# Performance work log

Hardware: AMD Instinct MI355X
Metric: run time of the kernel (lower is better)

## Reference

```python
import jax, jax.numpy as jnp
import numpy as np

TILE = 128
NEG = -1e10


def rotate_half(x):
    half = x.shape[-1] // 2
    return jnp.concatenate([-x[..., half:], x[..., :half]], axis=-1)


def setup_inputs() -> dict:
    key = jax.random.key(0)
    ks = jax.random.split(key, 7)
    B, S, E, H, D, K = 1, 4096, 2048, 16, 128, 8
    T = S // TILE
    x = jax.random.normal(ks[0], (B, S, E), jnp.float32)
    wq = jax.random.normal(ks[1], (E, H * D), jnp.float32) * 0.02
    wk = jax.random.normal(ks[2], (E, H * D), jnp.float32) * 0.02
    wv = jax.random.normal(ks[3], (E, H * D), jnp.float32) * 0.02
    wo = jax.random.normal(ks[4], (H * D, E), jnp.float32) * 0.02
    rope_angles = jax.random.uniform(ks[5], (S, D // 2), jnp.float32)
    anchor_indices = jax.random.randint(ks[6], (B, H, T, K), 0, T).astype(jnp.int32)
    return {"x": x, "wq": wq, "wk": wk, "wv": wv, "wo": wo,
            "rope_angles": rope_angles, "anchor_indices": anchor_indices}


def reference(x, wq, wk, wv, wo, rope_angles, anchor_indices):
    B, S, E = x.shape
    D = rope_angles.shape[1] * 2          # head_dim
    H = wq.shape[1] // D                  # num_heads
    T = S // TILE                         # num_tiles
    sm_scale = 1.0 / jnp.sqrt(jnp.float32(D))

    # QKV projections -> [B, H, S, D]
    def proj(w):
        return (x @ w).reshape(B, S, H, D).transpose(0, 2, 1, 3).astype(jnp.float32)
    q, k, v = proj(wq), proj(wk), proj(wv)

    # RoPE (half-split / rotate_half format)
    cos = jnp.cos(rope_angles)[None, None]   # [1,1,S,D/2]
    sin = jnp.sin(rope_angles)[None, None]
    cos_f = jnp.concatenate([cos, cos], axis=-1)
    sin_f = jnp.concatenate([sin, sin], axis=-1)
    q = q * cos_f + rotate_half(q) * sin_f
    k = k * cos_f + rotate_half(k) * sin_f

    # Tile selection: anchor tiles + local (diagonal) tile -> [B,H,T,K+1]
    local = jnp.broadcast_to(jnp.arange(T, dtype=jnp.int32)[None, None, :, None], (B, H, T, 1))
    tile_sel = jnp.concatenate([anchor_indices, local], axis=-1)
    L = tile_sel.shape[-1] * TILE            # sparse_len
    token_idx = tile_sel[..., None] * TILE + jnp.arange(TILE, dtype=jnp.int32)[None, None, None, None, :]
    flat_idx = jnp.clip(token_idx.reshape(B, H, T, L), 0, S - 1)  # [B,H,T,L]

    # Gather selected KV tiles: [B,H,T,L,D]
    def gather(kv):
        return jnp.take_along_axis(kv, flat_idx.reshape(B, H, T * L, 1), axis=2).reshape(B, H, T, L, D)
    k_sp, v_sp = gather(k), gather(v)

    # Block-sparse attention per query tile
    q_t = q.reshape(B, H, T, TILE, D)
    logits = jnp.einsum('bhtqd,bhtkd->bhtqk', q_t, k_sp) * sm_scale
    q_pos = jnp.arange(S).reshape(T, TILE)
    future = flat_idx[:, :, :, None, :] > q_pos[None, None, :, :, None]  # causal mask on gathered keys
    logits = jnp.where(future, NEG, logits)
    w = jax.nn.softmax(logits, axis=-1)
    all_masked = jnp.all(future, axis=-1, keepdims=True)
    w = jnp.where(all_masked, 0.0, w)
    w = jnp.where(jnp.isnan(w), 0.0, w)
    out = jnp.einsum('bhtqk,bhtkd->bhtqd', w, v_sp)

    out = out.reshape(B, H, S, D).transpose(0, 2, 1, 3).reshape(B, S, H * D)
    return out @ wo
```

## Files before the change

### kernel.cpp

```cpp
#include <hip/hip_runtime.h>
#include <stdint.h>

typedef unsigned short u16;
typedef unsigned int u32;

#define S_LEN 4096
#define EMB 2048
#define NH 16
#define HD 128
#define HDTOT 2048
#define T_TILES 32
#define KANCH 8
#define SM_SCALE 0.088388347648318447f

typedef __bf16 bf16x8 __attribute__((ext_vector_type(8)));
typedef float f32x4 __attribute__((ext_vector_type(4)));

typedef const __attribute__((address_space(1))) u32 ga_u32;
typedef __attribute__((address_space(3))) u32 lds_u32;

__device__ __forceinline__ u16 f2bf(float f) {
  u32 b = __builtin_bit_cast(u32, f);
  b = (b + 0x7FFFu + ((b >> 16) & 1u)) >> 16;
  return (u16)b;
}
__device__ __forceinline__ float bf2f(u16 u) {
  return __builtin_bit_cast(float, ((u32)u) << 16);
}
__device__ __forceinline__ f32x4 mfma16(bf16x8 a, bf16x8 b, f32x4 c) {
  return __builtin_amdgcn_mfma_f32_16x16x32_bf16(a, b, c, 0, 0, 0);
}

__global__ __launch_bounds__(256) void k_convert_x(const float* __restrict__ x,
                                                   u16* __restrict__ xb) {
  int i = (blockIdx.x * 256 + threadIdx.x) * 4;
  float4 v = *(const float4*)(x + i);
  ushort4 o;
  o.x = f2bf(v.x); o.y = f2bf(v.y); o.z = f2bf(v.z); o.w = f2bf(v.w);
  *(ushort4*)(xb + i) = o;
}

__global__ __launch_bounds__(256) void k_transpose_w(
    const float* __restrict__ w0, const float* __restrict__ w1,
    const float* __restrict__ w2, const float* __restrict__ w3,
    u16* __restrict__ o0, u16* __restrict__ o1,
    u16* __restrict__ o2, u16* __restrict__ o3) {
  const float* w; u16* o;
  if (blockIdx.z == 0)      { w = w0; o = o0; }
  else if (blockIdx.z == 1) { w = w1; o = o1; }
  else if (blockIdx.z == 2) { w = w2; o = o2; }
  else                      { w = w3; o = o3; }
  __shared__ float tile[64][68];
  int n0 = blockIdx.x * 64, k0 = blockIdx.y * 64;
  int tid = threadIdx.x;
  int r = tid >> 4, cq = (tid & 15) << 2;
  for (int p = 0; p < 4; ++p) {
    float4 v = *(const float4*)(w + (size_t)(k0 + r + p * 16) * EMB + n0 + cq);
    tile[r + p * 16][cq + 0] = v.x;
    tile[r + p * 16][cq + 1] = v.y;
    tile[r + p * 16][cq + 2] = v.z;
    tile[r + p * 16][cq + 3] = v.w;
  }
  __syncthreads();
  for (int p = 0; p < 4; ++p) {
    int rn = r + p * 16;
    ushort4 u;
    u.x = f2bf(tile[cq + 0][rn]);
    u.y = f2bf(tile[cq + 1][rn]);
    u.z = f2bf(tile[cq + 2][rn]);
    u.w = f2bf(tile[cq + 3][rn]);
    *(ushort4*)(o + (size_t)(n0 + rn) * EMB + k0 + cq) = u;
  }
}

__global__ __launch_bounds__(256) void k_transpose_v(const u16* __restrict__ v,
                                                     u16* __restrict__ vt) {
  __shared__ u16 tile[64][72];
  int n0 = blockIdx.x * 64, s0 = blockIdx.y * 64;
  int tid = threadIdx.x;
  int r = tid >> 4, cq = (tid & 15) << 2;
  for (int p = 0; p < 4; ++p) {
    ushort4 u = *(const ushort4*)(v + (size_t)(s0 + r + p * 16) * HDTOT + n0 + cq);
    tile[r + p * 16][cq + 0] = u.x;
    tile[r + p * 16][cq + 1] = u.y;
    tile[r + p * 16][cq + 2] = u.z;
    tile[r + p * 16][cq + 3] = u.w;
  }
  __syncthreads();
  for (int p = 0; p < 4; ++p) {
    int rn = r + p * 16;
    ushort4 o;
    o.x = tile[cq + 0][rn];
    o.y = tile[cq + 1][rn];
    o.z = tile[cq + 2][rn];
    o.w = tile[cq + 3][rn];
    *(ushort4*)(vt + (size_t)(n0 + rn) * S_LEN + s0 + cq) = o;
  }
}

template <bool BF16OUT>
__device__ __forceinline__ void gemm_body(const u16* __restrict__ A,
                                          const u16* __restrict__ Bt,
                                          void* __restrict__ Cv,
                                          int N, int K, int m0, int n0,
                                          u16* As, u16* Bs) {
  const int tid = threadIdx.x;
  const int lane = tid & 63, wave = tid >> 6;
  const int quad = lane >> 4, l16 = lane & 15;
  const int wm = (wave >> 1) * 64, wn = (wave & 1) * 64;
  f32x4 acc[4][4] = {};

  const int flat0 = wave * 1024 + lane * 16;
  for (int kt = 0; kt < K; kt += 32) {
    for (int half = 0; half < 2; ++half) {
      int flat = flat0 + half * 4096;
      int row = flat >> 6, colb = flat & 63;
      const char* ga = (const char*)A + ((size_t)(m0 + row) * K + kt) * 2 + colb;
      const char* gb = (const char*)Bt + ((size_t)(n0 + row) * K + kt) * 2 + colb;
      int loff = wave * 1024 + half * 4096;
      __builtin_amdgcn_global_load_lds((ga_u32*)ga, (lds_u32*)((char*)As + loff), 16, 0, 0);
      __builtin_amdgcn_global_load_lds((ga_u32*)gb, (lds_u32*)((char*)Bs + loff), 16, 0, 0);
    }
    __syncthreads();
    bf16x8 af[4], bfr[4];
    for (int mt = 0; mt < 4; ++mt)
      af[mt] = *(const bf16x8*)(As + (wm + mt * 16 + l16) * 32 + quad * 8);
    for (int nt = 0; nt < 4; ++nt)
      bfr[nt] = *(const bf16x8*)(Bs + (wn + nt * 16 + l16) * 32 + quad * 8);
    for (int mt = 0; mt < 4; ++mt)
      for (int nt = 0; nt < 4; ++nt)
        acc[mt][nt] = mfma16(af[mt], bfr[nt], acc[mt][nt]);
    __syncthreads();
  }
  for (int mt = 0; mt < 4; ++mt) {
    int row = m0 + wm + mt * 16 + quad * 4;
    for (int nt = 0; nt < 4; ++nt) {
      int col = n0 + wn + nt * 16 + l16;
      for (int r = 0; r < 4; ++r) {
        if (BF16OUT)
          ((u16*)Cv)[(size_t)(row + r) * N + col] = f2bf(acc[mt][nt][r]);
        else
          ((float*)Cv)[(size_t)(row + r) * N + col] = acc[mt][nt][r];
      }
    }
  }
}

template <bool BF16OUT>
__global__ __launch_bounds__(256) void k_gemm(const u16* __restrict__ A,
                                              const u16* __restrict__ Bt,
                                              void* __restrict__ Cv,
                                              int N, int K) {
  __shared__ __align__(16) u16 As[128 * 32];
  __shared__ __align__(16) u16 Bs[128 * 32];
  gemm_body<BF16OUT>(A, Bt, Cv, N, K, blockIdx.y * 128, blockIdx.x * 128, As, Bs);
}

__global__ __launch_bounds__(256) void k_gemm_qkv(const u16* __restrict__ A,
                                                  const u16* __restrict__ Bt,
                                                  u16* __restrict__ q,
                                                  u16* __restrict__ k,
                                                  u16* __restrict__ v) {
  __shared__ __align__(16) u16 As[128 * 32];
  __shared__ __align__(16) u16 Bs[128 * 32];
  const int nb = blockIdx.x;
  u16* out = (nb < 16) ? q : ((nb < 32) ? k : v);
  gemm_body<true>(A, Bt + (size_t)((nb >> 4) * 2048) * EMB, out,
                  HDTOT, EMB, blockIdx.y * 128, (nb & 15) * 128, As, Bs);
}

__global__ __launch_bounds__(256) void k_rope(u16* __restrict__ q, u16* __restrict__ k,
                                              const float* __restrict__ ang) {
  int gid = blockIdx.x * 256 + threadIdx.x;
  int s = gid >> 10;
  int h = (gid >> 6) & (NH - 1);
  int d = gid & 63;
  float a = ang[s * 64 + d];
  float sn, cs;
  __sincosf(a, &sn, &cs);
  size_t base = (size_t)s * HDTOT + h * HD + d;
  float q1 = bf2f(q[base]), q2 = bf2f(q[base + 64]);
  q[base] = f2bf(q1 * cs - q2 * sn);
  q[base + 64] = f2bf(q2 * cs + q1 * sn);
  float k1 = bf2f(k[base]), k2 = bf2f(k[base + 64]);
  k[base] = f2bf(k1 * cs - k2 * sn);
  k[base + 64] = f2bf(k2 * cs + k1 * sn);
}

__device__ __forceinline__ bf16x8 ldsfrag(const u16* __restrict__ sbuf, int r, int cb) {
  return *(const bf16x8*)(sbuf + r * 128 + (((cb ^ (r & 15)) << 3)));
}

__global__ __launch_bounds__(512, 1) void k_attn(const u16* __restrict__ q,
                                                 const u16* __restrict__ k,
                                                 const u16* __restrict__ vt,
                                                 const int* __restrict__ anch,
                                                 u16* __restrict__ out) {
  __shared__ __align__(16) u16 bufK[2][128 * 128];
  __shared__ __align__(16) u16 bufV[2][128 * 128];
  __shared__ int s_tj[KANCH + 1];
  __shared__ int s_nv;
  const int t = T_TILES - 1 - blockIdx.x;
  const int h = blockIdx.y;
  const int tid = threadIdx.x;
  const int lane = tid & 63, wave = tid >> 6;
  const int quad = lane >> 4, l16 = lane & 15;
  const int wq0 = wave * 16;

  int offK[4], offV[4];
#pragma unroll
  for (int p = 0; p < 4; ++p) {
    int row = (wave * 4 + p) * 4 + (lane >> 4);
    int colsw = ((lane & 15) ^ (row & 15)) << 3;
    offK[p] = (row * HDTOT + colsw) * 2;
    offV[p] = (row * S_LEN + colsw) * 2;
  }

  if (tid == 0) {
    int nv = 0;
    for (int j = 0; j < KANCH; ++j) {
      int tj = anch[((h * T_TILES) + t) * KANCH + j];
      if (tj <= t) s_tj[nv++] = tj;
    }
    s_tj[nv++] = t;
    s_nv = nv;
  }

  {
    const char* gq = (const char*)(q + (size_t)(t * 128) * HDTOT + h * HD);
    char* lq = (char*)bufV[1] + wave * 4096;
#pragma unroll
    for (int p = 0; p < 4; ++p)
      __builtin_amdgcn_global_load_lds((ga_u32*)(gq + offK[p]),
                                       (lds_u32*)(lq + p * 1024), 16, 0, 0);
  }
  __syncthreads();

  bf16x8 qf[4];
#pragma unroll
  for (int ks = 0; ks < 4; ++ks)
    qf[ks] = ldsfrag(bufV[1], wq0 + l16, ks * 4 + quad);

  const int nv = s_nv;
  const char* kh = (const char*)(k + h * HD);
  const char* vh = (const char*)(vt + (size_t)(h * HD) * S_LEN);

  {
    int tj0 = s_tj[0];
    const char* gk = kh + (size_t)(tj0 * 128) * (HDTOT * 2);
    const char* gv = vh + (size_t)(tj0 * 128) * 2;
    char* lk = (char*)bufK[0] + wave * 4096;
    char* lv = (char*)bufV[0] + wave * 4096;
#pragma unroll
    for (int p = 0; p < 4; ++p) {
      __builtin_amdgcn_global_load_lds((ga_u32*)(gk + offK[p]),
                                       (lds_u32*)(lk + p * 1024), 16, 0, 0);
      __builtin_amdgcn_global_load_lds((ga_u32*)(gv + offV[p]),
                                       (lds_u32*)(lv + p * 1024), 16, 0, 0);
    }
  }

  f32x4 oacc[8] = {};
  float m_st = -1e30f, l_st = 0.f;

  for (int i = 0; i < nv; ++i) {
    const int par = i & 1;
    const u16* K_c = bufK[par];
    const u16* V_c = bufV[par];
    const int tj = s_tj[i];
    const bool diag = (tj == t);

    __syncthreads();

    if (i + 1 < nv) {
      int tjn = s_tj[i + 1];
      const char* gk = kh + (size_t)(tjn * 128) * (HDTOT * 2);
      const char* gv = vh + (size_t)(tjn * 128) * 2;
      char* lk = (char*)bufK[1 - par] + wave * 4096;
      char* lv = (char*)bufV[1 - par] + wave * 4096;
#pragma unroll
      for (int p = 0; p < 4; ++p) {
        __builtin_amdgcn_global_load_lds((ga_u32*)(gk + offK[p]),
                                         (lds_u32*)(lk + p * 1024), 16, 0, 0);
        __builtin_amdgcn_global_load_lds((ga_u32*)(gv + offV[p]),
                                         (lds_u32*)(lv + p * 1024), 16, 0, 0);
      }
    }

    f32x4 sacc[8] = {};
#pragma unroll
    for (int ks = 0; ks < 4; ++ks)
#pragma unroll
      for (int a = 0; a < 8; ++a) {
        bf16x8 kf = ldsfrag(K_c, a * 16 + l16, ks * 4 + quad);
        sacc[a] = mfma16(kf, qf[ks], sacc[a]);
      }

    u32 pl[8], ph[8];
    float alpha;
    {
      const int qr = wq0 + l16;
      float rmax = -1e30f;
#pragma unroll
      for (int a = 0; a < 8; ++a) {
        f32x4 s4 = sacc[a];
#pragma unroll
        for (int r = 0; r < 4; ++r) {
          float sv = s4[r] * SM_SCALE;
          if (diag && (a * 16 + quad * 4 + r > qr)) sv = -1e30f;
          s4[r] = sv;
          rmax = fmaxf(rmax, sv);
        }
        sacc[a] = s4;
      }
      rmax = fmaxf(rmax, __shfl_xor(rmax, 16));
      rmax = fmaxf(rmax, __shfl_xor(rmax, 32));
      float mnew = fmaxf(m_st, rmax);
      alpha = __expf(m_st - mnew);
      m_st = mnew;
      float rsum = 0.f;
#pragma unroll
      for (int a = 0; a < 8; ++a) {
        f32x4 s4 = sacc[a];
        float p0 = __expf(s4[0] - mnew);
        float p1 = __expf(s4[1] - mnew);
        float p2 = __expf(s4[2] - mnew);
        float p3 = __expf(s4[3] - mnew);
        rsum += (p0 + p1) + (p2 + p3);
        pl[a] = __builtin_amdgcn_perm(__builtin_bit_cast(u32, p1) + 0x8000u,
                                      __builtin_bit_cast(u32, p0) + 0x8000u,
                                      0x07060302u);
        ph[a] = __builtin_amdgcn_perm(__builtin_bit_cast(u32, p3) + 0x8000u,
                                      __builtin_bit_cast(u32, p2) + 0x8000u,
                                      0x07060302u);
      }
      rsum += __shfl_xor(rsum, 16);
      rsum += __shfl_xor(rsum, 32);
      l_st = l_st * alpha + rsum;
    }

    {
      f32x4 av;
#pragma unroll
      for (int r = 0; r < 4; ++r)
        av[r] = __shfl(alpha, (lane & 48) | (quad * 4 + r));
#pragma unroll
      for (int nt = 0; nt < 8; ++nt) {
        f32x4 o4 = oacc[nt];
        o4[0] *= av[0]; o4[1] *= av[1]; o4[2] *= av[2]; o4[3] *= av[3];
        oacc[nt] = o4;
      }
    }

    const int srcA = ((quad & 1) << 5) + l16;
    const int srcB = srcA + 16;
    const int hi = quad >> 1;
#pragma unroll
    for (int c = 0; c < 4; ++c) {
      u32 x0 = __shfl(pl[2 * c], srcA), x1 = __shfl(ph[2 * c], srcA);
      u32 x2 = __shfl(pl[2 * c], srcB), x3 = __shfl(ph[2 * c], srcB);
      u32 y0 = __shfl(pl[2 * c + 1], srcA), y1 = __shfl(ph[2 * c + 1], srcA);
      u32 y2 = __shfl(pl[2 * c + 1], srcB), y3 = __shfl(ph[2 * c + 1], srcB);
      uint4 w;
      w.x = hi ? y0 : x0;
      w.y = hi ? y1 : x1;
      w.z = hi ? y2 : x2;
      w.w = hi ? y3 : x3;
      bf16x8 pa = __builtin_bit_cast(bf16x8, w);
#pragma unroll
      for (int nt = 0; nt < 8; ++nt) {
        bf16x8 vf = ldsfrag(V_c, nt * 16 + l16, c * 4 + quad);
        oacc[nt] = mfma16(pa, vf, oacc[nt]);
      }
    }
  }

  {
    float linv = 1.0f / l_st;
    f32x4 iv;
#pragma unroll
    for (int r = 0; r < 4; ++r)
      iv[r] = __shfl(linv, (lane & 48) | (quad * 4 + r));
#pragma unroll
    for (int r = 0; r < 4; ++r) {
      size_t srow_o = (size_t)(t * 128 + wq0 + quad * 4 + r);
#pragma unroll
      for (int nt = 0; nt < 8; ++nt)
        out[srow_o * HDTOT + h * HD + nt * 16 + l16] = f2bf(oacc[nt][r] * iv[r]);
    }
  }
}

extern "C" void kernel_launch(void* const* d_in, const int* in_sizes, int n_in,
                              void* d_out, int out_size, void* d_ws, size_t ws_size,
                              hipStream_t stream) {
  const float* x   = (const float*)d_in[0];
  const float* wq  = (const float*)d_in[1];
  const float* wk  = (const float*)d_in[2];
  const float* wv  = (const float*)d_in[3];
  const float* wo  = (const float*)d_in[4];
  const float* ang = (const float*)d_in[5];
  const int* anch  = (const int*)d_in[6];

  char* ws = (char*)d_ws;
  const size_t SZ_SE = (size_t)S_LEN * HDTOT * sizeof(u16);
  const size_t SZ_W  = (size_t)EMB * EMB * sizeof(u16);
  u16* xb   = (u16*)(ws);
  u16* qb   = (u16*)(ws + SZ_SE);
  u16* kb   = (u16*)(ws + 2 * SZ_SE);
  u16* vb   = (u16*)(ws + 3 * SZ_SE);
  u16* vtb  = (u16*)(ws + 4 * SZ_SE);
  u16* attn = (u16*)(ws + 5 * SZ_SE);
  u16* wqT  = (u16*)(ws + 6 * SZ_SE);
  u16* wkT  = (u16*)(ws + 6 * SZ_SE + SZ_W);
  u16* wvT  = (u16*)(ws + 6 * SZ_SE + 2 * SZ_W);
  u16* woT  = (u16*)(ws + 6 * SZ_SE + 3 * SZ_W);

  k_convert_x<<<8192, 256, 0, stream>>>(x, xb);
  k_transpose_w<<<dim3(32, 32, 4), 256, 0, stream>>>(wq, wk, wv, wo, wqT, wkT, wvT, woT);
  k_gemm_qkv<<<dim3(48, 32), 256, 0, stream>>>(xb, wqT, qb, kb, vb);
  k_rope<<<16384, 256, 0, stream>>>(qb, kb, ang);
  k_transpose_v<<<dim3(32, 64), 256, 0, stream>>>(vb, vtb);
  k_attn<<<dim3(T_TILES, NH), 512, 0, stream>>>(qb, kb, vtb, anch, attn);
  k_gemm<false><<<dim3(16, 32), 256, 0, stream>>>(attn, woT, d_out, EMB, HDTOT);
}
```

Before: 411.1 us.

## Halve attention KV tile to 64 keys for occupancy; vectorize RoPE kernel

The attention kernel now streams each 128-key KV tile as two 64-key halves. This halves the LDS buffers from 128KB to 64KB and raises launch bounds to allow up to 4 blocks per CU, with an adjusted V swizzle and a diag mask offset. The RoPE kernel processes 8 elements per thread with vectorized loads and stores, cutting its grid eightfold. The cost is twice as many loop iterations and barriers per tile, plus extra online-softmax rescaling steps. The grid is only 512 blocks, so higher occupancy may not help much.

Measured after the change: 401.0 us. 2.5% less time.

```diff
diff --git a/kernel.cpp b/kernel.cpp
--- a/kernel.cpp
+++ b/kernel.cpp
@@ -172,32 +172,60 @@
 __global__ __launch_bounds__(256) void k_rope(u16* __restrict__ q, u16* __restrict__ k,
                                               const float* __restrict__ ang) {
   int gid = blockIdx.x * 256 + threadIdx.x;
-  int s = gid >> 10;
-  int h = (gid >> 6) & (NH - 1);
-  int d = gid & 63;
-  float a = ang[s * 64 + d];
-  float sn, cs;
-  __sincosf(a, &sn, &cs);
-  size_t base = (size_t)s * HDTOT + h * HD + d;
-  float q1 = bf2f(q[base]), q2 = bf2f(q[base + 64]);
-  q[base] = f2bf(q1 * cs - q2 * sn);
-  q[base + 64] = f2bf(q2 * cs + q1 * sn);
-  float k1 = bf2f(k[base]), k2 = bf2f(k[base + 64]);
-  k[base] = f2bf(k1 * cs - k2 * sn);
-  k[base + 64] = f2bf(k2 * cs + k1 * sn);
+  int s = gid >> 7;
+  int h = (gid >> 3) & (NH - 1);
+  int dq = (gid & 7) << 3;
+  const float* ap = ang + s * 64 + dq;
+  float4 a0 = *(const float4*)(ap);
+  float4 a1 = *(const float4*)(ap + 4);
+  float sn[8], cs[8];
+  __sincosf(a0.x, &sn[0], &cs[0]);
+  __sincosf(a0.y, &sn[1], &cs[1]);
+  __sincosf(a0.z, &sn[2], &cs[2]);
+  __sincosf(a0.w, &sn[3], &cs[3]);
+  __sincosf(a1.x, &sn[4], &cs[4]);
+  __sincosf(a1.y, &sn[5], &cs[5]);
+  __sincosf(a1.z, &sn[6], &cs[6]);
+  __sincosf(a1.w, &sn[7], &cs[7]);
+  size_t base = (size_t)s * HDTOT + h * HD + dq;
+  u16* ptrs[2] = {q, k};
+#pragma unroll
+  for (int a = 0; a < 2; ++a) {
+    u16* p = ptrs[a] + base;
+    ushort4 x1a = *(const ushort4*)(p);
+    ushort4 x1b = *(const ushort4*)(p + 4);
+    ushort4 x2a = *(const ushort4*)(p + 64);
+    ushort4 x2b = *(const ushort4*)(p + 68);
+    u16 v1[8] = {x1a.x, x1a.y, x1a.z, x1a.w, x1b.x, x1b.y, x1b.z, x1b.w};
+    u16 v2[8] = {x2a.x, x2a.y, x2a.z, x2a.w, x2b.x, x2b.y, x2b.z, x2b.w};
+    u16 o1[8], o2[8];
+#pragma unroll
+    for (int e = 0; e < 8; ++e) {
+      float f1 = bf2f(v1[e]), f2 = bf2f(v2[e]);
+      o1[e] = f2bf(f1 * cs[e] - f2 * sn[e]);
+      o2[e] = f2bf(f2 * cs[e] + f1 * sn[e]);
+    }
+    *(ushort4*)(p)      = make_ushort4(o1[0], o1[1], o1[2], o1[3]);
+    *(ushort4*)(p + 4)  = make_ushort4(o1[4], o1[5], o1[6], o1[7]);
+    *(ushort4*)(p + 64) = make_ushort4(o2[0], o2[1], o2[2], o2[3]);
+    *(ushort4*)(p + 68) = make_ushort4(o2[4], o2[5], o2[6], o2[7]);
+  }
 }
 
 __device__ __forceinline__ bf16x8 ldsfrag(const u16* __restrict__ sbuf, int r, int cb) {
   return *(const bf16x8*)(sbuf + r * 128 + (((cb ^ (r & 15)) << 3)));
 }
-
-__global__ __launch_bounds__(512, 1) void k_attn(const u16* __restrict__ q,
+__device__ __forceinline__ bf16x8 ldsfragV(const u16* __restrict__ sbuf, int r, int cb) {
+  return *(const bf16x8*)(sbuf + r * 64 + (((cb ^ (r & 7)) << 3)));
+}
+
+__global__ __launch_bounds__(512, 4) void k_attn(const u16* __restrict__ q,
                                                  const u16* __restrict__ k,
                                                  const u16* __restrict__ vt,
                                                  const int* __restrict__ anch,
                                                  u16* __restrict__ out) {
-  __shared__ __align__(16) u16 bufK[2][128 * 128];
-  __shared__ __align__(16) u16 bufV[2][128 * 128];
+  __shared__ __align__(16) u16 bufK[2][64 * 128];
+  __shared__ __align__(16) u16 bufV[2][128 * 64];
   __shared__ int s_tj[KANCH + 1];
   __shared__ int s_nv;
   const int t = T_TILES - 1 - blockIdx.x;
@@ -207,13 +235,15 @@
   const int quad = lane >> 4, l16 = lane & 15;
   const int wq0 = wave * 16;
 
-  int offK[4], offV[4];
-#pragma unroll
-  for (int p = 0; p < 4; ++p) {
-    int row = (wave * 4 + p) * 4 + (lane >> 4);
-    int colsw = ((lane & 15) ^ (row & 15)) << 3;
-    offK[p] = (row * HDTOT + colsw) * 2;
-    offV[p] = (row * S_LEN + colsw) * 2;
+  int offK[2], offV[2];
+#pragma unroll
+  for (int p = 0; p < 2; ++p) {
+    int krow = (wave * 2 + p) * 4 + (lane >> 4);
+    int kcol = ((lane & 15) ^ (krow & 15)) << 3;
+    offK[p] = (krow * HDTOT + kcol) * 2;
+    int vrow = (wave * 2 + p) * 8 + (lane >> 3);
+    int vcol = ((lane & 7) ^ (vrow & 7)) << 3;
+    offV[p] = (vrow * S_LEN + vcol) * 2;
   }
 
   if (tid == 0) {
@@ -228,31 +258,36 @@
 
   {
     const char* gq = (const char*)(q + (size_t)(t * 128) * HDTOT + h * HD);
-    char* lq = (char*)bufV[1] + wave * 4096;
-#pragma unroll
-    for (int p = 0; p < 4; ++p)
-      __builtin_amdgcn_global_load_lds((ga_u32*)(gq + offK[p]),
+    char* lq = (char*)bufK + wave * 4096;
+#pragma unroll
+    for (int p = 0; p < 4; ++p) {
+      int qrow = (wave * 4 + p) * 4 + (lane >> 4);
+      int qcol = ((lane & 15) ^ (qrow & 15)) << 3;
+      __builtin_amdgcn_global_load_lds((ga_u32*)(gq + (qrow * HDTOT + qcol) * 2),
                                        (lds_u32*)(lq + p * 1024), 16, 0, 0);
+    }
   }
   __syncthreads();
 
   bf16x8 qf[4];
 #pragma unroll
   for (int ks = 0; ks < 4; ++ks)
-    qf[ks] = ldsfrag(bufV[1], wq0 + l16, ks * 4 + quad);
-
-  const int nv = s_nv;
+    qf[ks] = ldsfrag(&bufK[0][0], wq0 + l16, ks * 4 + quad);
+
+  const int nv2 = 2 * s_nv;
   const char* kh = (const char*)(k + h * HD);
   const char* vh = (const char*)(vt + (size_t)(h * HD) * S_LEN);
 
+  __syncthreads();
+
   {
-    int tj0 = s_tj[0];
-    const char* gk = kh + (size_t)(tj0 * 128) * (HDTOT * 2);
-    const char* gv = vh + (size_t)(tj0 * 128) * 2;
-    char* lk = (char*)bufK[0] + wave * 4096;
-    char* lv = (char*)bufV[0] + wave * 4096;
-#pragma unroll
-    for (int p = 0; p < 4; ++p) {
+    int key0 = s_tj[0] * 128;
+    const char* gk = kh + (size_t)key0 * (HDTOT * 2);
+    const char* gv = vh + (size_t)key0 * 2;
+    char* lk = (char*)bufK[0] + wave * 2048;
+    char* lv = (char*)bufV[0] + wave * 2048;
+#pragma unroll
+    for (int p = 0; p < 2; ++p) {
       __builtin_amdgcn_global_load_lds((ga_u32*)(gk + offK[p]),
                                        (lds_u32*)(lk + p * 1024), 16, 0, 0);
       __builtin_amdgcn_global_load_lds((ga_u32*)(gv + offV[p]),
@@ -263,23 +298,25 @@
   f32x4 oacc[8] = {};
   float m_st = -1e30f, l_st = 0.f;
 
-  for (int i = 0; i < nv; ++i) {
+  for (int i = 0; i < nv2; ++i) {
     const int par = i & 1;
     const u16* K_c = bufK[par];
     const u16* V_c = bufV[par];
-    const int tj = s_tj[i];
+    const int tj = s_tj[i >> 1];
+    const int half = i & 1;
     const bool diag = (tj == t);
 
     __syncthreads();
 
-    if (i + 1 < nv) {
-      int tjn = s_tj[i + 1];
-      const char* gk = kh + (size_t)(tjn * 128) * (HDTOT * 2);
-      const char* gv = vh + (size_t)(tjn * 128) * 2;
-      char* lk = (char*)bufK[1 - par] + wave * 4096;
-      char* lv = (char*)bufV[1 - par] + wave * 4096;
-#pragma unroll
-      for (int p = 0; p < 4; ++p) {
+    if (i + 1 < nv2) {
+      int inx = i + 1;
+      int key0 = s_tj[inx >> 1] * 128 + (inx & 1) * 64;
+      const char* gk = kh + (size_t)key0 * (HDTOT * 2);
+      const char* gv = vh + (size_t)key0 * 2;
+      char* lk = (char*)bufK[1 - par] + wave * 2048;
+      char* lv = (char*)bufV[1 - par] + wave * 2048;
+#pragma unroll
+      for (int p = 0; p < 2; ++p) {
         __builtin_amdgcn_global_load_lds((ga_u32*)(gk + offK[p]),
                                          (lds_u32*)(lk + p * 1024), 16, 0, 0);
         __builtin_amdgcn_global_load_lds((ga_u32*)(gv + offV[p]),
@@ -287,27 +324,28 @@
       }
     }
 
-    f32x4 sacc[8] = {};
+    f32x4 sacc[4] = {};
 #pragma unroll
     for (int ks = 0; ks < 4; ++ks)
 #pragma unroll
-      for (int a = 0; a < 8; ++a) {
+      for (int a = 0; a < 4; ++a) {
         bf16x8 kf = ldsfrag(K_c, a * 16 + l16, ks * 4 + quad);
         sacc[a] = mfma16(kf, qf[ks], sacc[a]);
       }
 
-    u32 pl[8], ph[8];
+    u32 pl[4], ph[4];
     float alpha;
     {
       const int qr = wq0 + l16;
+      const int kb = half * 64;
       float rmax = -1e30f;
 #pragma unroll
-      for (int a = 0; a < 8; ++a) {
+      for (int a = 0; a < 4; ++a) {
         f32x4 s4 = sacc[a];
 #pragma unroll
         for (int r = 0; r < 4; ++r) {
           float sv = s4[r] * SM_SCALE;
-          if (diag && (a * 16 + quad * 4 + r > qr)) sv = -1e30f;
+          if (diag && (kb + a * 16 + quad * 4 + r > qr)) sv = -1e30f;
           s4[r] = sv;
           rmax = fmaxf(rmax, sv);
         }
@@ -320,7 +358,7 @@
       m_st = mnew;
       float rsum = 0.f;
 #pragma unroll
-      for (int a = 0; a < 8; ++a) {
+      for (int a = 0; a < 4; ++a) {
         f32x4 s4 = sacc[a];
         float p0 = __expf(s4[0] - mnew);
         float p1 = __expf(s4[1] - mnew);
@@ -356,7 +394,7 @@
     const int srcB = srcA + 16;
     const int hi = quad >> 1;
 #pragma unroll
-    for (int c = 0; c < 4; ++c) {
+    for (int c = 0; c < 2; ++c) {
       u32 x0 = __shfl(pl[2 * c], srcA), x1 = __shfl(ph[2 * c], srcA);
       u32 x2 = __shfl(pl[2 * c], srcB), x3 = __shfl(ph[2 * c], srcB);
       u32 y0 = __shfl(pl[2 * c + 1], srcA), y1 = __shfl(ph[2 * c + 1], srcA);
@@ -369,7 +407,7 @@
       bf16x8 pa = __builtin_bit_cast(bf16x8, w);
 #pragma unroll
       for (int nt = 0; nt < 8; ++nt) {
-        bf16x8 vf = ldsfrag(V_c, nt * 16 + l16, c * 4 + quad);
+        bf16x8 vf = ldsfragV(V_c, nt * 16 + l16, c * 4 + quad);
         oacc[nt] = mfma16(pa, vf, oacc[nt]);
       }
     }
@@ -419,7 +457,7 @@
   k_convert_x<<<8192, 256, 0, stream>>>(x, xb);
   k_transpose_w<<<dim3(32, 32, 4), 256, 0, stream>>>(wq, wk, wv, wo, wqT, wkT, wvT, woT);
   k_gemm_qkv<<<dim3(48, 32), 256, 0, stream>>>(xb, wqT, qb, kb, vb);
-  k_rope<<<16384, 256, 0, stream>>>(qb, kb, ang);
+  k_rope<<<2048, 256, 0, stream>>>(qb, kb, ang);
   k_transpose_v<<<dim3(32, 64), 256, 0, stream>>>(vb, vtb);
   k_attn<<<dim3(T_TILES, NH), 512, 0, stream>>>(qb, kb, vtb, anch, attn);
   k_gemm<false><<<dim3(16, 32), 256, 0, stream>>>(attn, woT, d_out, EMB, HDTOT);
```
